# Kernel tuning notes

Hardware: AMD Instinct MI355X
Metric: run time of the kernel (lower is better)

Reference implementation:

```python
import jax, jax.numpy as jnp
import numpy as np

POOL_SIZE = 7
CROP = POOL_SIZE * 2  # if_max_pool=True -> crop to 14x14 then 2x2 max-pool


def setup_inputs() -> dict:
    key = jax.random.key(0)
    k1, k2, k3 = jax.random.split(key, 3)
    H, W, C = 50, 75, 512          # VGG conv5 features of an 800x1200 image (stride 16)
    N = 1000                       # post-NMS RPN proposals
    feature_map = jax.random.normal(k1, (1, H, W, C), dtype=jnp.float32)
    img_size = jnp.array([800, 1200], dtype=jnp.int32)
    # rois in pixel coords (x1, y1, x2, y2), guaranteed x1<=x2, y1<=y2, in-bounds
    xs = jax.random.uniform(k2, (N, 2), minval=0.0, maxval=1199.0)
    ys = jax.random.uniform(k3, (N, 2), minval=0.0, maxval=799.0)
    rois = jnp.stack([xs.min(1), ys.min(1), xs.max(1), ys.max(1)], axis=1).astype(jnp.float32)
    return {"feature_map": feature_map, "rois": rois, "img_size": img_size}


def _crop_and_resize(feature_map, boxes, crop_h, crop_w):
    """tf.image.crop_and_resize (bilinear) with all box_indices == 0.
    feature_map: (1,H,W,C); boxes: (N,4) normalized [y1,x1,y2,x2].
    Returns (N, crop_h, crop_w, C).
    """
    H, W = feature_map.shape[1], feature_map.shape[2]
    img = feature_map[0]  # (H,W,C)
    y1, x1, y2, x2 = boxes[:, 0], boxes[:, 1], boxes[:, 2], boxes[:, 3]
    fh, fw = jnp.float32(H - 1), jnp.float32(W - 1)
    iy = jnp.arange(crop_h, dtype=jnp.float32)
    ix = jnp.arange(crop_w, dtype=jnp.float32)
    # in-image sample coords (crop size > 1 branch of TF semantics)
    ys = y1[:, None] * fh + iy[None, :] * ((y2 - y1) * fh / (crop_h - 1))[:, None]  # (N,ch)
    xs = x1[:, None] * fw + ix[None, :] * ((x2 - x1) * fw / (crop_w - 1))[:, None]  # (N,cw)
    valid = ((ys >= 0) & (ys <= fh))[:, :, None] & ((xs >= 0) & (xs <= fw))[:, None, :]  # (N,ch,cw)
    y0 = jnp.floor(ys); x0 = jnp.floor(xs)
    wy = (ys - y0)[:, :, None, None]   # (N,ch,1,1)
    wx = (xs - x0)[:, None, :, None]   # (N,1,cw,1)
    y0i = jnp.clip(y0.astype(jnp.int32), 0, H - 1)
    x0i = jnp.clip(x0.astype(jnp.int32), 0, W - 1)
    y1i = jnp.clip(y0i + 1, 0, H - 1)
    x1i = jnp.clip(x0i + 1, 0, W - 1)
    # per-ROI bilinear gather: (N,ch,cw,C)
    tl = img[y0i[:, :, None], x0i[:, None, :]]
    tr = img[y0i[:, :, None], x1i[:, None, :]]
    bl = img[y1i[:, :, None], x0i[:, None, :]]
    br = img[y1i[:, :, None], x1i[:, None, :]]
    top = tl + wx * (tr - tl)
    bot = bl + wx * (br - bl)
    val = top + wy * (bot - top)
    return jnp.where(valid[..., None], val, 0.0)


def reference(feature_map, rois, img_size):
    img_h = img_size[0].astype(jnp.float32) - 1.0
    img_w = img_size[1].astype(jnp.float32) - 1.0
    boxes = jnp.stack([rois[:, 1] / img_h, rois[:, 0] / img_w,
                       rois[:, 3] / img_h, rois[:, 2] / img_w], axis=1)
    boxes = jax.lax.stop_gradient(boxes)
    crops = _crop_and_resize(feature_map, boxes, CROP, CROP)  # (N,14,14,C)
    N, _, _, C = crops.shape
    # MaxPool2D((2,2), padding='same'); 14 is even so 'same' == 'valid' reshape trick
    return crops.reshape(N, POOL_SIZE, 2, POOL_SIZE, 2, C).max(axis=(2, 4))
```

## Files before the change

kernel.cpp:

```cpp
#include <hip/hip_runtime.h>

#define FH 50
#define FW 75
#define FC 512
#define NPOOL 7

__global__ __launch_bounds__(128) void roi_pool_kernel(
    const float* __restrict__ fmap,
    const float* __restrict__ rois,
    const int*   __restrict__ img_size,
    float* __restrict__ out,
    int N)
{
    int bid = blockIdx.x;
    int n  = bid / (NPOOL * NPOOL);
    int p  = bid % (NPOOL * NPOOL);
    int py = p / NPOOL;
    int px = p % NPOOL;
    if (n >= N) return;

    const float img_h = (float)(img_size[0] - 1);
    const float img_w = (float)(img_size[1] - 1);

    const float rx1 = rois[n * 4 + 0];
    const float ry1 = rois[n * 4 + 1];
    const float rx2 = rois[n * 4 + 2];
    const float ry2 = rois[n * 4 + 3];
    const float by1 = ry1 / img_h;
    const float bx1 = rx1 / img_w;
    const float by2 = ry2 / img_h;
    const float bx2 = rx2 / img_w;

    const float fh = (float)(FH - 1);
    const float fw = (float)(FW - 1);
    const float stepy = (by2 - by1) * fh * (1.0f / 13.0f);
    const float stepx = (bx2 - bx1) * fw * (1.0f / 13.0f);
    const float basey = by1 * fh;
    const float basex = bx1 * fw;

    const int t  = threadIdx.x;
    const int c4 = t * 4;

    float4 m = make_float4(-INFINITY, -INFINITY, -INFINITY, -INFINITY);

    #pragma unroll
    for (int kk = 0; kk < 4; ++kk) {
        const int iy = py * 2 + (kk >> 1);
        const int ix = px * 2 + (kk & 1);
        const float ys = basey + (float)iy * stepy;
        const float xs = basex + (float)ix * stepx;
        const bool valid = (ys >= 0.0f) & (ys <= fh) & (xs >= 0.0f) & (xs <= fw);

        const float y0f = floorf(ys);
        const float x0f = floorf(xs);
        const float wy = ys - y0f;
        const float wx = xs - x0f;
        int y0i = (int)y0f; y0i = min(max(y0i, 0), FH - 1);
        int x0i = (int)x0f; x0i = min(max(x0i, 0), FW - 1);
        const int y1i = min(y0i + 1, FH - 1);
        const int x1i = min(x0i + 1, FW - 1);

        const float4 tl = *(const float4*)(fmap + ((long)y0i * FW + x0i) * FC + c4);
        const float4 tr = *(const float4*)(fmap + ((long)y0i * FW + x1i) * FC + c4);
        const float4 bl = *(const float4*)(fmap + ((long)y1i * FW + x0i) * FC + c4);
        const float4 br = *(const float4*)(fmap + ((long)y1i * FW + x1i) * FC + c4);

        float4 val;
        {
            float top, bot;
            top = tl.x + wx * (tr.x - tl.x);
            bot = bl.x + wx * (br.x - bl.x);
            val.x = top + wy * (bot - top);
            top = tl.y + wx * (tr.y - tl.y);
            bot = bl.y + wx * (br.y - bl.y);
            val.y = top + wy * (bot - top);
            top = tl.z + wx * (tr.z - tl.z);
            bot = bl.z + wx * (br.z - bl.z);
            val.z = top + wy * (bot - top);
            top = tl.w + wx * (tr.w - tl.w);
            bot = bl.w + wx * (br.w - bl.w);
            val.w = top + wy * (bot - top);
        }
        if (!valid) { val.x = 0.0f; val.y = 0.0f; val.z = 0.0f; val.w = 0.0f; }

        m.x = fmaxf(m.x, val.x);
        m.y = fmaxf(m.y, val.y);
        m.z = fmaxf(m.z, val.z);
        m.w = fmaxf(m.w, val.w);
    }

    float4* dst = (float4*)(out + (((long)n * NPOOL + py) * NPOOL + px) * FC + c4);
    *dst = m;
}

extern "C" void kernel_launch(void* const* d_in, const int* in_sizes, int n_in,
                              void* d_out, int out_size, void* d_ws, size_t ws_size,
                              hipStream_t stream) {
    const float* fmap     = (const float*)d_in[0];
    const float* rois     = (const float*)d_in[1];
    const int*   img_size = (const int*)d_in[2];
    float* out = (float*)d_out;

    const int N = in_sizes[1] / 4;
    const int blocks = N * NPOOL * NPOOL;
    roi_pool_kernel<<<blocks, 128, 0, stream>>>(fmap, rois, img_size, out, N);
}
```

Baseline: 168.8 us.

## Process a full pooled row per block with XCD-aware block remapping

```diff
diff --git a/kernel.cpp b/kernel.cpp
--- a/kernel.cpp
+++ b/kernel.cpp
@@ -4,6 +4,13 @@
 #define FW 75
 #define FC 512
 #define NPOOL 7
+#define NXCD 8
+
+typedef float f32x4 __attribute__((ext_vector_type(4)));
+
+__device__ __forceinline__ float uniform_f(float x) {
+    return __int_as_float(__builtin_amdgcn_readfirstlane(__float_as_int(x)));
+}
 
 __global__ __launch_bounds__(128) void roi_pool_kernel(
     const float* __restrict__ fmap,
@@ -12,11 +19,13 @@
     float* __restrict__ out,
     int N)
 {
-    int bid = blockIdx.x;
-    int n  = bid / (NPOOL * NPOOL);
-    int p  = bid % (NPOOL * NPOOL);
-    int py = p / NPOOL;
-    int px = p % NPOOL;
+    const int nwg = gridDim.x;
+    const int q = nwg / NXCD, r = nwg % NXCD;
+    const int xcd = blockIdx.x % NXCD, local = blockIdx.x / NXCD;
+    const int w = (xcd < r ? xcd * (q + 1) : r * (q + 1) + (xcd - r) * q) + local;
+
+    const int n  = w / NPOOL;
+    const int py = w % NPOOL;
     if (n >= N) return;
 
     const float img_h = (float)(img_size[0] - 1);
@@ -26,71 +35,91 @@
     const float ry1 = rois[n * 4 + 1];
     const float rx2 = rois[n * 4 + 2];
     const float ry2 = rois[n * 4 + 3];
-    const float by1 = ry1 / img_h;
-    const float bx1 = rx1 / img_w;
-    const float by2 = ry2 / img_h;
-    const float bx2 = rx2 / img_w;
 
     const float fh = (float)(FH - 1);
     const float fw = (float)(FW - 1);
-    const float stepy = (by2 - by1) * fh * (1.0f / 13.0f);
-    const float stepx = (bx2 - bx1) * fw * (1.0f / 13.0f);
-    const float basey = by1 * fh;
-    const float basex = bx1 * fw;
+    const float stepy = (ry2 - ry1) / img_h * fh * (1.0f / 13.0f);
+    const float stepx = (rx2 - rx1) / img_w * fw * (1.0f / 13.0f);
+    const float basey = ry1 / img_h * fh;
+    const float basex = rx1 / img_w * fw;
 
-    const int t  = threadIdx.x;
-    const int c4 = t * 4;
+    float wy[2]; float my[2]; int roff[2][2];
+    #pragma unroll
+    for (int i = 0; i < 2; ++i) {
+        const int iy = py * 2 + i;
+        const float ys = basey + (float)iy * stepy;
+        my[i] = ((ys >= 0.0f) & (ys <= fh)) ? 1.0f : 0.0f;
+        const float y0f = floorf(ys);
+        wy[i] = uniform_f(ys - y0f);
+        my[i] = uniform_f(my[i]);
+        int y0 = min(max((int)y0f, 0), FH - 1);
+        int y1 = min(y0 + 1, FH - 1);
+        roff[i][0] = __builtin_amdgcn_readfirstlane(y0 * (FW * FC));
+        roff[i][1] = __builtin_amdgcn_readfirstlane(y1 * (FW * FC));
+    }
+    float wx[14]; float mx[14]; int coff[14][2];
+    #pragma unroll
+    for (int j = 0; j < 14; ++j) {
+        const float xs = basex + (float)j * stepx;
+        mx[j] = ((xs >= 0.0f) & (xs <= fw)) ? 1.0f : 0.0f;
+        const float x0f = floorf(xs);
+        wx[j] = uniform_f(xs - x0f);
+        mx[j] = uniform_f(mx[j]);
+        int x0 = min(max((int)x0f, 0), FW - 1);
+        int x1 = min(x0 + 1, FW - 1);
+        coff[j][0] = __builtin_amdgcn_readfirstlane(x0 * FC);
+        coff[j][1] = __builtin_amdgcn_readfirstlane(x1 * FC);
+    }
 
-    float4 m = make_float4(-INFINITY, -INFINITY, -INFINITY, -INFINITY);
+    const int c4 = threadIdx.x * 4;
+    const float* fm = fmap + c4;
+    float* orow = out + ((long)(n * NPOOL + py) * NPOOL) * FC + c4;
 
     #pragma unroll
-    for (int kk = 0; kk < 4; ++kk) {
-        const int iy = py * 2 + (kk >> 1);
-        const int ix = px * 2 + (kk & 1);
-        const float ys = basey + (float)iy * stepy;
-        const float xs = basex + (float)ix * stepx;
-        const bool valid = (ys >= 0.0f) & (ys <= fh) & (xs >= 0.0f) & (xs <= fw);
+    for (int px = 0; px < NPOOL; ++px) {
+        const int j0 = px * 2, j1 = px * 2 + 1;
 
-        const float y0f = floorf(ys);
-        const float x0f = floorf(xs);
-        const float wy = ys - y0f;
-        const float wx = xs - x0f;
-        int y0i = (int)y0f; y0i = min(max(y0i, 0), FH - 1);
-        int x0i = (int)x0f; x0i = min(max(x0i, 0), FW - 1);
-        const int y1i = min(y0i + 1, FH - 1);
-        const int x1i = min(x0i + 1, FW - 1);
+        const f32x4 tl00 = *(const f32x4*)(fm + roff[0][0] + coff[j0][0]);
+        const f32x4 tr00 = *(const f32x4*)(fm + roff[0][0] + coff[j0][1]);
+        const f32x4 bl00 = *(const f32x4*)(fm + roff[0][1] + coff[j0][0]);
+        const f32x4 br00 = *(const f32x4*)(fm + roff[0][1] + coff[j0][1]);
+        const f32x4 tl01 = *(const f32x4*)(fm + roff[0][0] + coff[j1][0]);
+        const f32x4 tr01 = *(const f32x4*)(fm + roff[0][0] + coff[j1][1]);
+        const f32x4 bl01 = *(const f32x4*)(fm + roff[0][1] + coff[j1][0]);
+        const f32x4 br01 = *(const f32x4*)(fm + roff[0][1] + coff[j1][1]);
+        const f32x4 tl10 = *(const f32x4*)(fm + roff[1][0] + coff[j0][0]);
+        const f32x4 tr10 = *(const f32x4*)(fm + roff[1][0] + coff[j0][1]);
+        const f32x4 bl10 = *(const f32x4*)(fm + roff[1][1] + coff[j0][0]);
+        const f32x4 br10 = *(const f32x4*)(fm + roff[1][1] + coff[j0][1]);
+        const f32x4 tl11 = *(const f32x4*)(fm + roff[1][0] + coff[j1][0]);
+        const f32x4 tr11 = *(const f32x4*)(fm + roff[1][0] + coff[j1][1]);
+        const f32x4 bl11 = *(const f32x4*)(fm + roff[1][1] + coff[j1][0]);
+        const f32x4 br11 = *(const f32x4*)(fm + roff[1][1] + coff[j1][1]);
 
-        const float4 tl = *(const float4*)(fmap + ((long)y0i * FW + x0i) * FC + c4);
-        const float4 tr = *(const float4*)(fmap + ((long)y0i * FW + x1i) * FC + c4);
-        const float4 bl = *(const float4*)(fmap + ((long)y1i * FW + x0i) * FC + c4);
-        const float4 br = *(const float4*)(fmap + ((long)y1i * FW + x1i) * FC + c4);
+        f32x4 m = (f32x4){-INFINITY, -INFINITY, -INFINITY, -INFINITY};
 
-        float4 val;
-        {
-            float top, bot;
-            top = tl.x + wx * (tr.x - tl.x);
-            bot = bl.x + wx * (br.x - bl.x);
-            val.x = top + wy * (bot - top);
-            top = tl.y + wx * (tr.y - tl.y);
-            bot = bl.y + wx * (br.y - bl.y);
-            val.y = top + wy * (bot - top);
-            top = tl.z + wx * (tr.z - tl.z);
-            bot = bl.z + wx * (br.z - bl.z);
-            val.z = top + wy * (bot - top);
-            top = tl.w + wx * (tr.w - tl.w);
-            bot = bl.w + wx * (br.w - bl.w);
-            val.w = top + wy * (bot - top);
+        #define SAMP(TL, TR, BL, BR, I, J)                                   \
+        {                                                                     \
+            const float wyv = wy[I], wxv = wx[J];                             \
+            const float mv  = my[I] * mx[J];                                  \
+            f32x4 top = TL + wxv * (TR - TL);                                 \
+            f32x4 bot = BL + wxv * (BR - BL);                                 \
+            f32x4 v = top + wyv * (bot - top);                                \
+            v *= mv;                                                          \
+            m.x = fmaxf(m.x, v.x);                                            \
+            m.y = fmaxf(m.y, v.y);                                            \
+            m.z = fmaxf(m.z, v.z);                                            \
+            m.w = fmaxf(m.w, v.w);                                            \
         }
-        if (!valid) { val.x = 0.0f; val.y = 0.0f; val.z = 0.0f; val.w = 0.0f; }
 
-        m.x = fmaxf(m.x, val.x);
-        m.y = fmaxf(m.y, val.y);
-        m.z = fmaxf(m.z, val.z);
-        m.w = fmaxf(m.w, val.w);
+        SAMP(tl00, tr00, bl00, br00, 0, j0)
+        SAMP(tl01, tr01, bl01, br01, 0, j1)
+        SAMP(tl10, tr10, bl10, br10, 1, j0)
+        SAMP(tl11, tr11, bl11, br11, 1, j1)
+        #undef SAMP
+
+        __builtin_nontemporal_store(m, (f32x4*)(orow + px * FC));
     }
-
-    float4* dst = (float4*)(out + (((long)n * NPOOL + py) * NPOOL + px) * FC + c4);
-    *dst = m;
 }
 
 extern "C" void kernel_launch(void* const* d_in, const int* in_sizes, int n_in,
@@ -102,6 +131,6 @@
     float* out = (float*)d_out;
 
     const int N = in_sizes[1] / 4;
-    const int blocks = N * NPOOL * NPOOL;
+    const int blocks = N * NPOOL;
     roi_pool_kernel<<<blocks, 128, 0, stream>>>(fmap, rois, img_size, out, N);
 }
```

Result: faster. 164.8 us (-2.3%).

## Stage bilinear taps via global_load_lds, remap blocks per XCD, nontemporal stores

Applied to the files above, without the earlier changes.

```diff
diff --git a/kernel.cpp b/kernel.cpp
--- a/kernel.cpp
+++ b/kernel.cpp
@@ -4,6 +4,16 @@
 #define FW 75
 #define FC 512
 #define NPOOL 7
+#define NXCD 8
+
+typedef float f32x4 __attribute__((ext_vector_type(4)));
+
+typedef const __attribute__((address_space(1))) void g_void;
+typedef __attribute__((address_space(3))) void l_void;
+
+__device__ __forceinline__ float uniform_f(float x) {
+    return __int_as_float(__builtin_amdgcn_readfirstlane(__float_as_int(x)));
+}
 
 __global__ __launch_bounds__(128) void roi_pool_kernel(
     const float* __restrict__ fmap,
@@ -12,11 +22,17 @@
     float* __restrict__ out,
     int N)
 {
-    int bid = blockIdx.x;
-    int n  = bid / (NPOOL * NPOOL);
-    int p  = bid % (NPOOL * NPOOL);
-    int py = p / NPOOL;
-    int px = p % NPOOL;
+    __shared__ float lds[16 * FC];
+
+    const int nwg = gridDim.x;
+    const int q = nwg / NXCD, r = nwg % NXCD;
+    const int xcd = blockIdx.x % NXCD, local = blockIdx.x / NXCD;
+    const int w = (xcd < r ? xcd * (q + 1) : r * (q + 1) + (xcd - r) * q) + local;
+
+    const int n  = w / (NPOOL * NPOOL);
+    const int p  = w % (NPOOL * NPOOL);
+    const int py = p / NPOOL;
+    const int px = p % NPOOL;
     if (n >= N) return;
 
     const float img_h = (float)(img_size[0] - 1);
@@ -26,23 +42,16 @@
     const float ry1 = rois[n * 4 + 1];
     const float rx2 = rois[n * 4 + 2];
     const float ry2 = rois[n * 4 + 3];
-    const float by1 = ry1 / img_h;
-    const float bx1 = rx1 / img_w;
-    const float by2 = ry2 / img_h;
-    const float bx2 = rx2 / img_w;
 
     const float fh = (float)(FH - 1);
     const float fw = (float)(FW - 1);
-    const float stepy = (by2 - by1) * fh * (1.0f / 13.0f);
-    const float stepx = (bx2 - bx1) * fw * (1.0f / 13.0f);
-    const float basey = by1 * fh;
-    const float basex = bx1 * fw;
+    const float stepy = (ry2 - ry1) / img_h * fh * (1.0f / 13.0f);
+    const float stepx = (rx2 - rx1) / img_w * fw * (1.0f / 13.0f);
+    const float basey = ry1 / img_h * fh;
+    const float basex = rx1 / img_w * fw;
 
-    const int t  = threadIdx.x;
-    const int c4 = t * 4;
-
-    float4 m = make_float4(-INFINITY, -INFINITY, -INFINITY, -INFINITY);
-
+    int   off[16];
+    float wy_[4], wx_[4], mv_[4];
     #pragma unroll
     for (int kk = 0; kk < 4; ++kk) {
         const int iy = py * 2 + (kk >> 1);
@@ -50,47 +59,56 @@
         const float ys = basey + (float)iy * stepy;
         const float xs = basex + (float)ix * stepx;
         const bool valid = (ys >= 0.0f) & (ys <= fh) & (xs >= 0.0f) & (xs <= fw);
+        mv_[kk] = uniform_f(valid ? 1.0f : 0.0f);
 
         const float y0f = floorf(ys);
         const float x0f = floorf(xs);
-        const float wy = ys - y0f;
-        const float wx = xs - x0f;
+        wy_[kk] = uniform_f(ys - y0f);
+        wx_[kk] = uniform_f(xs - x0f);
         int y0i = (int)y0f; y0i = min(max(y0i, 0), FH - 1);
         int x0i = (int)x0f; x0i = min(max(x0i, 0), FW - 1);
         const int y1i = min(y0i + 1, FH - 1);
         const int x1i = min(x0i + 1, FW - 1);
-
-        const float4 tl = *(const float4*)(fmap + ((long)y0i * FW + x0i) * FC + c4);
-        const float4 tr = *(const float4*)(fmap + ((long)y0i * FW + x1i) * FC + c4);
-        const float4 bl = *(const float4*)(fmap + ((long)y1i * FW + x0i) * FC + c4);
-        const float4 br = *(const float4*)(fmap + ((long)y1i * FW + x1i) * FC + c4);
-
-        float4 val;
-        {
-            float top, bot;
-            top = tl.x + wx * (tr.x - tl.x);
-            bot = bl.x + wx * (br.x - bl.x);
-            val.x = top + wy * (bot - top);
-            top = tl.y + wx * (tr.y - tl.y);
-            bot = bl.y + wx * (br.y - bl.y);
-            val.y = top + wy * (bot - top);
-            top = tl.z + wx * (tr.z - tl.z);
-            bot = bl.z + wx * (br.z - bl.z);
-            val.z = top + wy * (bot - top);
-            top = tl.w + wx * (tr.w - tl.w);
-            bot = bl.w + wx * (br.w - bl.w);
-            val.w = top + wy * (bot - top);
-        }
-        if (!valid) { val.x = 0.0f; val.y = 0.0f; val.z = 0.0f; val.w = 0.0f; }
-
-        m.x = fmaxf(m.x, val.x);
-        m.y = fmaxf(m.y, val.y);
-        m.z = fmaxf(m.z, val.z);
-        m.w = fmaxf(m.w, val.w);
+        off[kk * 4 + 0] = __builtin_amdgcn_readfirstlane((y0i * FW + x0i) * FC);
+        off[kk * 4 + 1] = __builtin_amdgcn_readfirstlane((y0i * FW + x1i) * FC);
+        off[kk * 4 + 2] = __builtin_amdgcn_readfirstlane((y1i * FW + x0i) * FC);
+        off[kk * 4 + 3] = __builtin_amdgcn_readfirstlane((y1i * FW + x1i) * FC);
     }
 
-    float4* dst = (float4*)(out + (((long)n * NPOOL + py) * NPOOL + px) * FC + c4);
-    *dst = m;
+    const int t  = threadIdx.x;
+    const int ch = t * 4;
+    const int wavebase = (t >> 6) << 8;
+
+    const float* src = fmap + ch;
+    #pragma unroll
+    for (int c = 0; c < 16; ++c) {
+        __builtin_amdgcn_global_load_lds(
+            (g_void*)(src + off[c]),
+            (l_void*)&lds[c * FC + wavebase],
+            16, 0, 0);
+    }
+    asm volatile("s_waitcnt vmcnt(0)" ::: "memory");
+
+    f32x4 m = (f32x4){-INFINITY, -INFINITY, -INFINITY, -INFINITY};
+    #pragma unroll
+    for (int kk = 0; kk < 4; ++kk) {
+        const f32x4 tl = *(const f32x4*)&lds[(kk * 4 + 0) * FC + ch];
+        const f32x4 tr = *(const f32x4*)&lds[(kk * 4 + 1) * FC + ch];
+        const f32x4 bl = *(const f32x4*)&lds[(kk * 4 + 2) * FC + ch];
+        const f32x4 br = *(const f32x4*)&lds[(kk * 4 + 3) * FC + ch];
+        const float wyv = wy_[kk], wxv = wx_[kk], mv = mv_[kk];
+        f32x4 top = tl + wxv * (tr - tl);
+        f32x4 bot = bl + wxv * (br - bl);
+        f32x4 v = top + wyv * (bot - top);
+        v *= mv;
+        m.x = fmaxf(m.x, v.x);
+        m.y = fmaxf(m.y, v.y);
+        m.z = fmaxf(m.z, v.z);
+        m.w = fmaxf(m.w, v.w);
+    }
+
+    f32x4* dst = (f32x4*)(out + (((long)n * NPOOL + py) * NPOOL + px) * FC + ch);
+    __builtin_nontemporal_store(m, dst);
 }
 
 extern "C" void kernel_launch(void* const* d_in, const int* in_sizes, int n_in,
```

Result: slower. 195.3 us (+15.7%).
